# Kernel optimization log

Measured on AMD Instinct MI355X. Metric: run time of the kernel, lower is better.

Reference implementation:

```python
import jax, jax.numpy as jnp
import numpy as np

N_QUBITS = 8
N_LAYERS = 2
BATCH = 16384
DIM = 2 ** N_QUBITS

# PauliZ sign table: Z[q, idx] = +1 if bit q of idx is 0 else -1 (qubit 0 = MSB,
# matching state axis ordering below).
_bits = (np.arange(DIM)[:, None] >> (N_QUBITS - 1 - np.arange(N_QUBITS))) & 1
Z_SIGNS = jnp.asarray((1 - 2 * _bits).T.astype(np.float32))  # (n_qubits, 2^n)


def _apply_1q(state, gates, q):
    """Apply batched single-qubit gate. state: (B,)+(2,)*n complex, gates: (B,2,2)."""
    s = jnp.moveaxis(state, 1 + q, -1)
    s = jnp.einsum('nab,...b->...a', gates, s.reshape(gates.shape[0], -1, 2).reshape(s.shape))
    # the einsum above: gates (B,2,2) broadcast over the intermediate axes
    return jnp.moveaxis(s, -1, 1 + q)


def _apply_1q_batched(state, gates, q):
    s = jnp.moveaxis(state, 1 + q, -1)          # (B, ..., 2)
    s = jnp.einsum('nab,n...b->n...a', gates, s)
    return jnp.moveaxis(s, -1, 1 + q)


def _apply_cnot(state, c, t):
    s = jnp.moveaxis(state, (1 + c, 1 + t), (-2, -1))  # (..., 2_ctrl, 2_tgt)
    s = jnp.concatenate([s[..., :1, :], s[..., 1:, ::-1]], axis=-2)  # flip target where ctrl=1
    return jnp.moveaxis(s, (-2, -1), (1 + c, 1 + t))


def _rx_gate(theta):
    """Batched RX(theta): (B,) -> (B,2,2) complex."""
    c = jnp.cos(theta / 2)
    s = -1j * jnp.sin(theta / 2)
    return jnp.stack([jnp.stack([c + 0j, s], -1), jnp.stack([s, c + 0j], -1)], -2)


def _rot_gate(phi, theta, omega):
    """PennyLane Rot(phi,theta,omega) = RZ(omega) RY(theta) RZ(phi). Batched (B,)->(B,2,2)."""
    c = jnp.cos(theta / 2)
    s = jnp.sin(theta / 2)
    ep = jnp.exp(-0.5j * (phi + omega))  # e^{-i(phi+omega)/2}
    em = jnp.exp(0.5j * (phi - omega))   # e^{ i(phi-omega)/2}
    m00 = ep * c
    m01 = -em * s
    m10 = jnp.conj(em) * s
    m11 = jnp.conj(ep) * c
    return jnp.stack([jnp.stack([m00, m01], -1), jnp.stack([m10, m11], -1)], -2)


def _circuit(inputs, hidden):
    B = inputs.shape[0]
    n = N_QUBITS
    state = jnp.zeros((B,) + (2,) * n, jnp.complex64)
    state = state.at[(slice(None),) + (0,) * n].set(1.0 + 0j)
    # AngleEmbedding: RX(inputs[:, q]) on each wire q
    for q in range(n):
        state = _apply_1q_batched(state, _rx_gate(inputs[:, q]), q)
    # n_layers calls of StronglyEntanglingLayers, each with 1 layer of weights
    for l in range(N_LAYERS):
        w = hidden[:, l, 0]  # (B, n_qubits, 3)
        for q in range(n):
            state = _apply_1q_batched(state, _rot_gate(w[:, q, 0], w[:, q, 1], w[:, q, 2]), q)
        for q in range(n):  # CNOT ring, range r = 1
            state = _apply_cnot(state, q, (q + 1) % n)
    probs = jnp.abs(state.reshape(B, DIM)) ** 2          # (B, 2^n)
    expvals = probs @ Z_SIGNS.T                          # (B, n_qubits) <Z_q>
    return jnp.tanh(expvals)


def setup_inputs() -> dict:
    key = jax.random.key(0)
    k1, k2 = jax.random.split(key)
    inputs = jax.random.normal(k1, (BATCH, N_QUBITS), dtype=jnp.float32)
    hidden = jax.random.normal(k2, (BATCH, N_LAYERS, 1, N_QUBITS, 3), dtype=jnp.float32)
    return {"inputs": inputs, "hidden": hidden}


def reference(inputs, hidden):
    h = _circuit(inputs, hidden)
    return (h, h)
```

## Files before the change

kernel.cpp:

```cpp
#include <hip/hip_runtime.h>
#include <math.h>


#define DEVINL __device__ __forceinline__

DEVINL void fast_sincos_half(float x, float& s, float& c) {
    const float r = x * 0.07957747154594767f;
    s = __builtin_amdgcn_sinf(r);
    c = __builtin_amdgcn_cosf(r);
}

DEVINL float fast_tanh(float x) {
    const float t = __builtin_amdgcn_exp2f(x * 2.8853900817779268f);
    return 1.0f - 2.0f * __builtin_amdgcn_rcpf(t + 1.0f);
}

DEVINL void cmul(float ar, float ai, float br, float bi, float& cr, float& ci) {
    cr = ar*br - ai*bi;
    ci = ar*bi + ai*br;
}
DEVINL void cmulc(float ar, float ai, float br, float bi, float& cr, float& ci) {
    cr = ar*br + ai*bi;
    ci = ar*bi - ai*br;
}

template<int CTRL>
DEVINL float dpp_perm(float x) {
    return __int_as_float(__builtin_amdgcn_update_dpp(
        __float_as_int(x), __float_as_int(x), CTRL, 0xF, 0xF, false));
}

template<int OFF>
DEVINL float swz(float x) {
    return __int_as_float(__builtin_amdgcn_ds_swizzle(__float_as_int(x), OFF));
}

DEVINL void qubit_vec(float x, float phi, float theta, float omega,
                      float& v0r, float& v0i, float& v1r, float& v1i)
{
    float s, c;   fast_sincos_half(x, s, c);
    float st, ct; fast_sincos_half(theta, st, ct);
    float sa, ca; fast_sincos_half(phi + omega, sa, ca);
    float sb, cb; fast_sincos_half(phi - omega, sb, cb);
    const float A = c*ct, B = s*st, C = c*st, D = s*ct;
    v0r = ca*A - sb*B;
    v0i = cb*B - sa*A;
    v1r = cb*C + sa*D;
    v1i = -(sb*C + ca*D);
}

__global__ __launch_bounds__(256, 8)
void qcirc_kernel(const float* __restrict__ inputs,
                  const float* __restrict__ hidden,
                  float* __restrict__ out, int B)
{
    __shared__ __align__(16) float lds[512];

    const int t  = threadIdx.x;
    const int e  = blockIdx.x * 8 + (t >> 5);
    if (e >= B) return;
    const int sl = t & 31;
    const int gb = t & 32;
    const int q  = sl & 7;
    const int eb = (t >> 5) * 64;
    const int sl0 = sl & 1, sl1 = (sl >> 1) & 1, sl2 = (sl >> 2) & 1,
              sl3 = (sl >> 3) & 1, sl4 = (sl >> 4) & 1;

    const float  x  = inputs[(size_t)e * 8 + q];
    const float* hb = hidden + (size_t)e * 48 + q * 3;
    const float ph1 = hb[0], th1 = hb[1], om1 = hb[2];
    const float ph2 = hb[24], th2 = hb[25];

    float ov0r, ov0i, ov1r, ov1i;
    qubit_vec(x, ph1, th1, om1, ov0r, ov0i, ov1r, ov1i);
    float s2o, c2o; fast_sincos_half(th2, s2o, c2o);
    const float ho = ph2 * 0.07957747154594767f;
    const float Ec = __builtin_amdgcn_cosf(ho);
    const float Es = __builtin_amdgcn_sinf(ho);
    const float Av = (q < 3) ? Ec : ho;
    const float Bv = (q < 3) ? Es : 0.f;

    if (sl < 8) {
        *(float4*)(lds + eb + q*8)     = make_float4(ov0r, ov0i, ov1r, ov1i);
        *(float4*)(lds + eb + q*8 + 4) = make_float4(c2o, s2o, Av, Bv);
    }

    const float4 r4v = *(const float4*)(lds + eb + 32);
    const float4 r5v = *(const float4*)(lds + eb + 40);
    const float4 r6v = *(const float4*)(lds + eb + 48);
    const float4 r7v = *(const float4*)(lds + eb + 56);
    const int s4 = sl3 ^ sl4, s5 = sl2 ^ sl3, s6 = sl1, s7 = sl0 ^ sl1;
    const float a4r = s4 ? r4v.z : r4v.x, a4i = s4 ? r4v.w : r4v.y;
    const float a5r = s5 ? r5v.z : r5v.x, a5i = s5 ? r5v.w : r5v.y;
    const float a6r = s6 ? r6v.z : r6v.x, a6i = s6 ? r6v.w : r6v.y;
    const float a7r = s7 ? r7v.z : r7v.x, a7i = s7 ? r7v.w : r7v.y;
    float Lr, Li, tr, ti;
    cmul(a4r, a4i, a5r, a5i, tr, ti);
    cmul(tr, ti, a6r, a6i, Lr, Li);
    cmul(Lr, Li, a7r, a7i, tr, ti); Lr = tr; Li = ti;

    {
        const float h3 = lds[eb + 3*8 + 6];
        const float h4 = lds[eb + 4*8 + 6];
        const float h5 = lds[eb + 5*8 + 6];
        const float h6 = lds[eb + 6*8 + 6];
        const float h7 = lds[eb + 7*8 + 6];
        const float lam = (sl4 ? h3 : -h3) + (sl3 ? h4 : -h4) + (sl2 ? h5 : -h5)
                        + ((sl1 ^ sl2) ? h6 : -h6) + ((sl0 ^ sl2) ? h7 : -h7);
        const float Pc = __builtin_amdgcn_cosf(lam);
        const float Ps = __builtin_amdgcn_sinf(lam);
        cmul(Lr, Li, Pc, Ps, tr, ti); Lr = tr; Li = ti;
    }

    const float2 E0 = *(const float2*)(lds + eb + 0*8 + 6);
    const float2 E1 = *(const float2*)(lds + eb + 1*8 + 6);
    const float2 E2 = *(const float2*)(lds + eb + 2*8 + 6);

    const float4 r0v = *(const float4*)(lds + eb + 0);
    const float4 r1v = *(const float4*)(lds + eb + 8);
    const float4 r2v = *(const float4*)(lds + eb + 16);
    const float4 r3v = *(const float4*)(lds + eb + 24);

    const int b01 = sl0 ^ sl2;
    const float w0r0 = b01 ? r0v.z : r0v.x, w0i0 = b01 ? r0v.w : r0v.y;
    const float w0r1 = b01 ? r0v.x : r0v.z, w0i1 = b01 ? r0v.y : r0v.w;
    const float w1r0 = b01 ? r1v.z : r1v.x, w1i0 = b01 ? r1v.w : r1v.y;
    const float w1r1 = b01 ? r1v.x : r1v.z, w1i1 = b01 ? r1v.y : r1v.w;
    const float w3r0 = sl4 ? r3v.z : r3v.x, w3i0 = sl4 ? r3v.w : r3v.y;
    const float w3r1 = sl4 ? r3v.x : r3v.z, w3i1 = sl4 ? r3v.y : r3v.w;

    float w3p0r, w3p0i, w3p1r, w3p1i;
    cmulc(E2.x, E2.y, w3r0, w3i0, w3p0r, w3p0i);
    cmul (w3r1, w3i1, E2.x, E2.y, w3p1r, w3p1i);

    float GL0r, GL0i, GL1r, GL1i, GL2r, GL2i, GL3r, GL3i;
    {
        const float a = E0.x*E1.x, b2 = E0.y*E1.y, c = E0.x*E1.y, d = E0.y*E1.x;
        const float P3r = a - b2, P3i = c + d;
        const float P1r = a + b2, P1i = c - d;
        cmulc(P3r, P3i, Lr, Li, GL0r, GL0i);
        cmul (P1r, P1i, Lr, Li, GL1r, GL1i);
        cmulc(P1r, P1i, Lr, Li, GL2r, GL2i);
        cmul (P3r, P3i, Lr, Li, GL3r, GL3i);
    }

    float T2r[4], T2i[4], T1r[4], T1i[4];
    cmul(w0r0, w0i0, w1r0, w1i0, tr, ti); cmul(tr, ti, GL0r, GL0i, T2r[0], T2i[0]);
    cmul(w0r0, w0i0, w1r1, w1i1, tr, ti); cmul(tr, ti, GL1r, GL1i, T2r[1], T2i[1]);
    cmul(w0r1, w0i1, w1r1, w1i1, tr, ti); cmul(tr, ti, GL2r, GL2i, T2r[2], T2i[2]);
    cmul(w0r1, w0i1, w1r0, w1i0, tr, ti); cmul(tr, ti, GL3r, GL3i, T2r[3], T2i[3]);
    cmul(r2v.x, r2v.y, w3p0r, w3p0i, T1r[0], T1i[0]);
    cmul(r2v.z, r2v.w, w3p1r, w3p1i, T1r[1], T1i[1]);
    cmul(r2v.z, r2v.w, w3p0r, w3p0i, T1r[2], T1i[2]);
    cmul(r2v.x, r2v.y, w3p1r, w3p1i, T1r[3], T1i[3]);

    {
        const float2 cs = *(const float2*)(lds + eb + 0*8 + 4);
        #pragma unroll
        for (int j = 0; j < 2; ++j) {
            const float lr = T2r[j], li = T2i[j], hr = T2r[j+2], hi = T2i[j+2];
            T2r[j]   = cs.x*lr - cs.y*hr;  T2i[j]   = cs.x*li - cs.y*hi;
            T2r[j+2] = cs.y*lr + cs.x*hr;  T2i[j+2] = cs.y*li + cs.x*hi;
        }
    }
    {
        const float2 cs = *(const float2*)(lds + eb + 2*8 + 4);
        #pragma unroll
        for (int j = 0; j < 4; j += 2) {
            const float lr = T1r[j], li = T1i[j], hr = T1r[j+1], hi = T1i[j+1];
            T1r[j]   = cs.x*lr - cs.y*hr;  T1i[j]   = cs.x*li - cs.y*hi;
            T1r[j+1] = cs.y*lr + cs.x*hr;  T1i[j+1] = cs.y*li + cs.x*hi;
        }
    }

    float ar[8], ai[8];
    #pragma unroll
    for (int k = 0; k < 8; ++k)
        cmul(T2r[k >> 1], T2i[k >> 1], T1r[k & 3], T1i[k & 3], ar[k], ai[k]);

    {
        const float2 cs = *(const float2*)(lds + eb + 1*8 + 4);
        #pragma unroll
        for (int k0 = 0; k0 < 8; ++k0) {
            if (k0 & 2) continue;
            const int k1 = k0 | 2;
            const float lr = ar[k0], li = ai[k0], hr = ar[k1], hi = ai[k1];
            ar[k0] = cs.x*lr - cs.y*hr;  ai[k0] = cs.x*li - cs.y*hi;
            ar[k1] = cs.y*lr + cs.x*hr;  ai[k1] = cs.y*li + cs.x*hi;
        }
    }
    {
        const float2 cs = *(const float2*)(lds + eb + 3*8 + 4);
        const float se = sl4 ? cs.y : -cs.y;
        #pragma unroll
        for (int k = 0; k < 8; ++k) {
            const float pr = swz<0x401F>(ar[k]);
            const float pi = swz<0x401F>(ai[k]);
            ar[k] = cs.x*ar[k] + se*pr;
            ai[k] = cs.x*ai[k] + se*pi;
        }
    }
    {
        const float2 cs = *(const float2*)(lds + eb + 4*8 + 4);
        const float se = sl3 ? cs.y : -cs.y;
        #pragma unroll
        for (int k = 0; k < 8; ++k) {
            ar[k] = cs.x*ar[k] + se*dpp_perm<0x128>(ar[k]);
            ai[k] = cs.x*ai[k] + se*dpp_perm<0x128>(ai[k]);
        }
    }
    {
        const float2 cs = *(const float2*)(lds + eb + 5*8 + 4);
        const float se = sl2 ? cs.y : -cs.y;
        #pragma unroll
        for (int k = 0; k < 8; ++k) {
            ar[k] = cs.x*ar[k] + se*dpp_perm<0x141>(ar[k]);
            ai[k] = cs.x*ai[k] + se*dpp_perm<0x141>(ai[k]);
        }
    }
    {
        const float2 cs = *(const float2*)(lds + eb + 6*8 + 4);
        const float se = (sl1 ^ sl2) ? cs.y : -cs.y;
        #pragma unroll
        for (int k = 0; k < 8; ++k) {
            ar[k] = cs.x*ar[k] + se*dpp_perm<0x4E>(ar[k]);
            ai[k] = cs.x*ai[k] + se*dpp_perm<0x4E>(ai[k]);
        }
    }
    {
        const float2 cs = *(const float2*)(lds + eb + 7*8 + 4);
        const float se = (sl0 ^ sl2) ? cs.y : -cs.y;
        #pragma unroll
        for (int k = 0; k < 8; ++k) {
            ar[k] = cs.x*ar[k] + se*dpp_perm<0xB1>(ar[k]);
            ai[k] = cs.x*ai[k] + se*dpp_perm<0xB1>(ai[k]);
        }
    }

    float P[8];
    #pragma unroll
    for (int k = 0; k < 8; ++k) P[k] = ar[k]*ar[k] + ai[k]*ai[k];
    const float u0 = P[0]+P[1], v0 = P[0]-P[1];
    const float u1 = P[2]+P[3], v1 = P[2]-P[3];
    const float u2 = P[4]+P[5], v2 = P[4]-P[5];
    const float u3 = P[6]+P[7], v3 = P[6]-P[7];
    float V3 = v0 - v1 + v2 - v3;
    float V6 = u0 - u1 - u2 + u3;
    float V7 = v0 - v1 - v2 + v3;

    {
        const float g1 = (sl & 1) ? -1.f : 1.f;
        V3 = fmaf(g1, V3, dpp_perm<0xB1>(V3));
        V6 = fmaf(g1, V6, dpp_perm<0xB1>(V6));
        V7 = fmaf(g1, V7, dpp_perm<0xB1>(V7));
        const float g2 = (sl & 2) ? -1.f : 1.f;
        V3 = fmaf(g2, V3, dpp_perm<0x4E>(V3));
        V6 = fmaf(g2, V6, dpp_perm<0x4E>(V6));
        V7 = fmaf(g2, V7, dpp_perm<0x4E>(V7));
        const float g4 = (sl & 4) ? -1.f : 1.f;
        V3 = fmaf(g4, V3, swz<0x101F>(V3));
        V6 = fmaf(g4, V6, swz<0x101F>(V6));
        V7 = fmaf(g4, V7, swz<0x101F>(V7));
        const float g8 = (sl & 8) ? -1.f : 1.f;
        V3 = fmaf(g8, V3, dpp_perm<0x128>(V3));
        V6 = fmaf(g8, V6, dpp_perm<0x128>(V6));
        V7 = fmaf(g8, V7, dpp_perm<0x128>(V7));
        const float g16 = (sl & 16) ? -1.f : 1.f;
        V3 = fmaf(g16, V3, swz<0x401F>(V3));
        V6 = fmaf(g16, V6, swz<0x401F>(V6));
        V7 = fmaf(g16, V7, swz<0x401F>(V7));
    }

    const int idx7 = (sl == 3) ? 16 : (sl == 4) ? 24 : (sl == 5) ? 28
                   : (sl == 6) ? 26 : (sl == 7) ? 31 : 0;
    const float B3 = swz<0x3E0>(V3);
    const float B6 = swz<0x000>(V6);
    const float B7 = __shfl(V7, gb + idx7, 64);
    const float rsel = (sl == 0) ? B3 : (sl == 1) ? B6 : B7;
    const float h = fast_tanh(rsel);
    if (sl < 8) {
        const size_t obase = (size_t)e * 8;
        out[obase + sl] = h;
        out[(size_t)B * 8 + obase + sl] = h;
    }
}

extern "C" void kernel_launch(void* const* d_in, const int* in_sizes, int n_in,
                              void* d_out, int out_size, void* d_ws, size_t ws_size,
                              hipStream_t stream)
{
    const float* inputs = (const float*)d_in[0];
    const float* hidden = (const float*)d_in[1];
    float* out = (float*)d_out;
    const int B = in_sizes[0] / 8;
    const int blocks = (B + 7) / 8;
    hipLaunchKernelGGL(qcirc_kernel, dim3(blocks), dim3(256), 0, stream,
                       inputs, hidden, out, B);
}
```

Measured before the change: 13.53 us.

## Map each batch element to 16 lanes holding 16 amplitudes per lane

Each circuit instance now runs on 16 lanes instead of 32, and each lane holds 16 complex amplitudes instead of 8. Qubit 3 is therefore applied in registers rather than through a cross-lane swizzle, and one butterfly stage of the final reduction disappears. The qubit-4 swizzle in the reduction becomes a pair of DPP ops, and the final result gather is reorganised to match. This halves the lanes per element and removes ds_swizzle traffic, at the cost of twice the registers per lane (launch bounds are lowered from 8 to 4 blocks) and possibly lower occupancy.

```diff
diff --git a/kernel.cpp b/kernel.cpp
--- a/kernel.cpp
+++ b/kernel.cpp
@@ -16,12 +16,10 @@
 }
 
 DEVINL void cmul(float ar, float ai, float br, float bi, float& cr, float& ci) {
-    cr = ar*br - ai*bi;
-    ci = ar*bi + ai*br;
+    cr = ar*br - ai*bi;  ci = ar*bi + ai*br;
 }
 DEVINL void cmulc(float ar, float ai, float br, float bi, float& cr, float& ci) {
-    cr = ar*br + ai*bi;
-    ci = ar*bi - ai*br;
+    cr = ar*br + ai*bi;  ci = ar*bi - ai*br;
 }
 
 template<int CTRL>
@@ -29,7 +27,6 @@
     return __int_as_float(__builtin_amdgcn_update_dpp(
         __float_as_int(x), __float_as_int(x), CTRL, 0xF, 0xF, false));
 }
-
 template<int OFF>
 DEVINL float swz(float x) {
     return __int_as_float(__builtin_amdgcn_ds_swizzle(__float_as_int(x), OFF));
@@ -43,28 +40,25 @@
     float sa, ca; fast_sincos_half(phi + omega, sa, ca);
     float sb, cb; fast_sincos_half(phi - omega, sb, cb);
     const float A = c*ct, B = s*st, C = c*st, D = s*ct;
-    v0r = ca*A - sb*B;
-    v0i = cb*B - sa*A;
-    v1r = cb*C + sa*D;
-    v1i = -(sb*C + ca*D);
-}
-
-__global__ __launch_bounds__(256, 8)
+    v0r = ca*A - sb*B;  v0i = cb*B - sa*A;
+    v1r = cb*C + sa*D;  v1i = -(sb*C + ca*D);
+}
+
+__global__ __launch_bounds__(256, 4)
 void qcirc_kernel(const float* __restrict__ inputs,
                   const float* __restrict__ hidden,
                   float* __restrict__ out, int B)
 {
-    __shared__ __align__(16) float lds[512];
+    __shared__ __align__(16) float lds[1024];
 
     const int t  = threadIdx.x;
-    const int e  = blockIdx.x * 8 + (t >> 5);
+    const int e  = blockIdx.x * 16 + (t >> 4);
     if (e >= B) return;
-    const int sl = t & 31;
-    const int gb = t & 32;
+    const int sl = t & 15;
     const int q  = sl & 7;
-    const int eb = (t >> 5) * 64;
+    const int eb = (t >> 4) * 64;
     const int sl0 = sl & 1, sl1 = (sl >> 1) & 1, sl2 = (sl >> 2) & 1,
-              sl3 = (sl >> 3) & 1, sl4 = (sl >> 4) & 1;
+              sl3 = (sl >> 3) & 1;
 
     const float  x  = inputs[(size_t)e * 8 + q];
     const float* hb = hidden + (size_t)e * 48 + q * 3;
@@ -77,134 +71,142 @@
     const float ho = ph2 * 0.07957747154594767f;
     const float Ec = __builtin_amdgcn_cosf(ho);
     const float Es = __builtin_amdgcn_sinf(ho);
-    const float Av = (q < 3) ? Ec : ho;
-    const float Bv = (q < 3) ? Es : 0.f;
+    const float Av = (q < 4) ? Ec : ho;
+    const float Bv = (q < 4) ? Es : 0.f;
 
     if (sl < 8) {
         *(float4*)(lds + eb + q*8)     = make_float4(ov0r, ov0i, ov1r, ov1i);
         *(float4*)(lds + eb + q*8 + 4) = make_float4(c2o, s2o, Av, Bv);
     }
 
-    const float4 r4v = *(const float4*)(lds + eb + 32);
-    const float4 r5v = *(const float4*)(lds + eb + 40);
-    const float4 r6v = *(const float4*)(lds + eb + 48);
-    const float4 r7v = *(const float4*)(lds + eb + 56);
-    const int s4 = sl3 ^ sl4, s5 = sl2 ^ sl3, s6 = sl1, s7 = sl0 ^ sl1;
-    const float a4r = s4 ? r4v.z : r4v.x, a4i = s4 ? r4v.w : r4v.y;
-    const float a5r = s5 ? r5v.z : r5v.x, a5i = s5 ? r5v.w : r5v.y;
-    const float a6r = s6 ? r6v.z : r6v.x, a6i = s6 ? r6v.w : r6v.y;
-    const float a7r = s7 ? r7v.z : r7v.x, a7i = s7 ? r7v.w : r7v.y;
-    float Lr, Li, tr, ti;
-    cmul(a4r, a4i, a5r, a5i, tr, ti);
-    cmul(tr, ti, a6r, a6i, Lr, Li);
-    cmul(Lr, Li, a7r, a7i, tr, ti); Lr = tr; Li = ti;
-
-    {
-        const float h3 = lds[eb + 3*8 + 6];
+    float Lr, Li;
+    {
+        const float4 r5 = *(const float4*)(lds + eb + 40);
+        const float4 r6 = *(const float4*)(lds + eb + 48);
+        const float4 r7 = *(const float4*)(lds + eb + 56);
+        const int s5 = sl2 ^ sl3, s6 = sl1, s7 = sl0 ^ sl1;
+        const float a5r = s5 ? r5.z : r5.x, a5i = s5 ? r5.w : r5.y;
+        const float a6r = s6 ? r6.z : r6.x, a6i = s6 ? r6.w : r6.y;
+        const float a7r = s7 ? r7.z : r7.x, a7i = s7 ? r7.w : r7.y;
+        float tr, ti;
+        cmul(a5r, a5i, a6r, a6i, tr, ti);
+        cmul(tr, ti, a7r, a7i, Lr, Li);
+    }
+    {
         const float h4 = lds[eb + 4*8 + 6];
         const float h5 = lds[eb + 5*8 + 6];
         const float h6 = lds[eb + 6*8 + 6];
         const float h7 = lds[eb + 7*8 + 6];
-        const float lam = (sl4 ? h3 : -h3) + (sl3 ? h4 : -h4) + (sl2 ? h5 : -h5)
+        const float lam = (sl3 ? h4 : -h4) + (sl2 ? h5 : -h5)
                         + ((sl1 ^ sl2) ? h6 : -h6) + ((sl0 ^ sl2) ? h7 : -h7);
         const float Pc = __builtin_amdgcn_cosf(lam);
         const float Ps = __builtin_amdgcn_sinf(lam);
-        cmul(Lr, Li, Pc, Ps, tr, ti); Lr = tr; Li = ti;
-    }
-
-    const float2 E0 = *(const float2*)(lds + eb + 0*8 + 6);
-    const float2 E1 = *(const float2*)(lds + eb + 1*8 + 6);
-    const float2 E2 = *(const float2*)(lds + eb + 2*8 + 6);
-
-    const float4 r0v = *(const float4*)(lds + eb + 0);
-    const float4 r1v = *(const float4*)(lds + eb + 8);
-    const float4 r2v = *(const float4*)(lds + eb + 16);
-    const float4 r3v = *(const float4*)(lds + eb + 24);
-
-    const int b01 = sl0 ^ sl2;
-    const float w0r0 = b01 ? r0v.z : r0v.x, w0i0 = b01 ? r0v.w : r0v.y;
-    const float w0r1 = b01 ? r0v.x : r0v.z, w0i1 = b01 ? r0v.y : r0v.w;
-    const float w1r0 = b01 ? r1v.z : r1v.x, w1i0 = b01 ? r1v.w : r1v.y;
-    const float w1r1 = b01 ? r1v.x : r1v.z, w1i1 = b01 ? r1v.y : r1v.w;
-    const float w3r0 = sl4 ? r3v.z : r3v.x, w3i0 = sl4 ? r3v.w : r3v.y;
-    const float w3r1 = sl4 ? r3v.x : r3v.z, w3i1 = sl4 ? r3v.y : r3v.w;
-
-    float w3p0r, w3p0i, w3p1r, w3p1i;
-    cmulc(E2.x, E2.y, w3r0, w3i0, w3p0r, w3p0i);
-    cmul (w3r1, w3i1, E2.x, E2.y, w3p1r, w3p1i);
-
-    float GL0r, GL0i, GL1r, GL1i, GL2r, GL2i, GL3r, GL3i;
-    {
-        const float a = E0.x*E1.x, b2 = E0.y*E1.y, c = E0.x*E1.y, d = E0.y*E1.x;
-        const float P3r = a - b2, P3i = c + d;
-        const float P1r = a + b2, P1i = c - d;
-        cmulc(P3r, P3i, Lr, Li, GL0r, GL0i);
-        cmul (P1r, P1i, Lr, Li, GL1r, GL1i);
-        cmulc(P1r, P1i, Lr, Li, GL2r, GL2i);
-        cmul (P3r, P3i, Lr, Li, GL3r, GL3i);
-    }
-
-    float T2r[4], T2i[4], T1r[4], T1i[4];
-    cmul(w0r0, w0i0, w1r0, w1i0, tr, ti); cmul(tr, ti, GL0r, GL0i, T2r[0], T2i[0]);
-    cmul(w0r0, w0i0, w1r1, w1i1, tr, ti); cmul(tr, ti, GL1r, GL1i, T2r[1], T2i[1]);
-    cmul(w0r1, w0i1, w1r1, w1i1, tr, ti); cmul(tr, ti, GL2r, GL2i, T2r[2], T2i[2]);
-    cmul(w0r1, w0i1, w1r0, w1i0, tr, ti); cmul(tr, ti, GL3r, GL3i, T2r[3], T2i[3]);
-    cmul(r2v.x, r2v.y, w3p0r, w3p0i, T1r[0], T1i[0]);
-    cmul(r2v.z, r2v.w, w3p1r, w3p1i, T1r[1], T1i[1]);
-    cmul(r2v.z, r2v.w, w3p0r, w3p0i, T1r[2], T1i[2]);
-    cmul(r2v.x, r2v.y, w3p1r, w3p1i, T1r[3], T1i[3]);
-
-    {
-        const float2 cs = *(const float2*)(lds + eb + 0*8 + 4);
+        float tr, ti; cmul(Lr, Li, Pc, Ps, tr, ti); Lr = tr; Li = ti;
+    }
+
+    float Ur[4], Ui[4];
+    {
+        const float4 r0 = *(const float4*)(lds + eb + 0);
+        const float4 r1 = *(const float4*)(lds + eb + 8);
+        const float2 E0 = *(const float2*)(lds + eb + 0*8 + 6);
+        const float2 E1 = *(const float2*)(lds + eb + 1*8 + 6);
+        const int b01 = sl0 ^ sl2;
+        const float w00r = b01 ? r0.z : r0.x, w00i = b01 ? r0.w : r0.y;
+        const float w01r = b01 ? r0.x : r0.z, w01i = b01 ? r0.y : r0.w;
+        const float w10r = b01 ? r1.z : r1.x, w10i = b01 ? r1.w : r1.y;
+        const float w11r = b01 ? r1.x : r1.z, w11i = b01 ? r1.y : r1.w;
+        const float aa = E0.x*E1.x, bb = E0.y*E1.y, cc = E0.x*E1.y, dd = E0.y*E1.x;
+        const float P3r = aa - bb, P3i = cc + dd;
+        const float P1r = aa + bb, P1i = cc - dd;
+        float tr, ti;
+        cmul(w00r,w00i, w10r,w10i, tr,ti); cmulc(P3r,P3i, tr,ti, Ur[0],Ui[0]);
+        cmul(w00r,w00i, w11r,w11i, tr,ti); cmul (P1r,P1i, tr,ti, Ur[1],Ui[1]);
+        cmul(w01r,w01i, w11r,w11i, tr,ti); cmulc(P1r,P1i, tr,ti, Ur[2],Ui[2]);
+        cmul(w01r,w01i, w10r,w10i, tr,ti); cmul (P3r,P3i, tr,ti, Ur[3],Ui[3]);
+        const float2 cs0 = *(const float2*)(lds + eb + 0*8 + 4);
         #pragma unroll
         for (int j = 0; j < 2; ++j) {
-            const float lr = T2r[j], li = T2i[j], hr = T2r[j+2], hi = T2i[j+2];
-            T2r[j]   = cs.x*lr - cs.y*hr;  T2i[j]   = cs.x*li - cs.y*hi;
-            T2r[j+2] = cs.y*lr + cs.x*hr;  T2i[j+2] = cs.y*li + cs.x*hi;
-        }
-    }
-    {
-        const float2 cs = *(const float2*)(lds + eb + 2*8 + 4);
+            const float lr = Ur[j], li = Ui[j], hr = Ur[j+2], hi = Ui[j+2];
+            Ur[j]   = cs0.x*lr - cs0.y*hr;  Ui[j]   = cs0.x*li - cs0.y*hi;
+            Ur[j+2] = cs0.y*lr + cs0.x*hr;  Ui[j+2] = cs0.y*li + cs0.x*hi;
+        }
+    }
+
+    float T2r[8], T2i[8];
+    {
+        const float4 r2 = *(const float4*)(lds + eb + 16);
+        #pragma unroll
+        for (int m = 0; m < 8; ++m) {
+            const int idx = (m & 1) ^ ((m >> 1) & 1);
+            const float vr = idx ? r2.z : r2.x;
+            const float vi = idx ? r2.w : r2.y;
+            cmul(Ur[m >> 1], Ui[m >> 1], vr, vi, T2r[m], T2i[m]);
+        }
+        const float2 cs1 = *(const float2*)(lds + eb + 1*8 + 4);
+        #pragma unroll
+        for (int m = 0; m < 8; ++m) {
+            if (m & 2) continue;
+            const int m1 = m | 2;
+            const float lr = T2r[m], li = T2i[m], hr = T2r[m1], hi = T2i[m1];
+            T2r[m]  = cs1.x*lr - cs1.y*hr;  T2i[m]  = cs1.x*li - cs1.y*hi;
+            T2r[m1] = cs1.y*lr + cs1.x*hr;  T2i[m1] = cs1.y*li + cs1.x*hi;
+        }
+    }
+
+    float T1r[4], T1i[4];
+    {
+        const float4 r3 = *(const float4*)(lds + eb + 24);
+        const float4 r4 = *(const float4*)(lds + eb + 32);
+        const float2 E2 = *(const float2*)(lds + eb + 2*8 + 6);
+        const float2 E3 = *(const float2*)(lds + eb + 3*8 + 6);
+        const float w40r = sl3 ? r4.z : r4.x, w40i = sl3 ? r4.w : r4.y;
+        const float w41r = sl3 ? r4.x : r4.z, w41i = sl3 ? r4.y : r4.w;
+        float D0r, D0i, D1r, D1i;
+        cmulc(E3.x, E3.y, w40r, w40i, D0r, D0i);
+        cmul (w41r, w41i, E3.x, E3.y, D1r, D1i);
+        float LD0r, LD0i, LD1r, LD1i;
+        cmul(D0r, D0i, Lr, Li, LD0r, LD0i);
+        cmul(D1r, D1i, Lr, Li, LD1r, LD1i);
+        float e00r,e00i, e01r,e01i, e10r,e10i, e11r,e11i;
+        cmulc(E2.x, E2.y, r3.x, r3.y, e00r, e00i);
+        cmulc(E2.x, E2.y, r3.z, r3.w, e01r, e01i);
+        cmul (r3.z, r3.w, E2.x, E2.y, e10r, e10i);
+        cmul (r3.x, r3.y, E2.x, E2.y, e11r, e11i);
+        cmul(e00r, e00i, LD0r, LD0i, T1r[0], T1i[0]);
+        cmul(e01r, e01i, LD1r, LD1i, T1r[1], T1i[1]);
+        cmul(e10r, e10i, LD0r, LD0i, T1r[2], T1i[2]);
+        cmul(e11r, e11i, LD1r, LD1i, T1r[3], T1i[3]);
+        const float2 cs3 = *(const float2*)(lds + eb + 3*8 + 4);
         #pragma unroll
         for (int j = 0; j < 4; j += 2) {
             const float lr = T1r[j], li = T1i[j], hr = T1r[j+1], hi = T1i[j+1];
-            T1r[j]   = cs.x*lr - cs.y*hr;  T1i[j]   = cs.x*li - cs.y*hi;
-            T1r[j+1] = cs.y*lr + cs.x*hr;  T1i[j+1] = cs.y*li + cs.x*hi;
-        }
-    }
-
-    float ar[8], ai[8];
+            T1r[j]   = cs3.x*lr - cs3.y*hr;  T1i[j]   = cs3.x*li - cs3.y*hi;
+            T1r[j+1] = cs3.y*lr + cs3.x*hr;  T1i[j+1] = cs3.y*li + cs3.x*hi;
+        }
+    }
+
+    float ar[16], ai[16];
     #pragma unroll
-    for (int k = 0; k < 8; ++k)
+    for (int k = 0; k < 16; ++k)
         cmul(T2r[k >> 1], T2i[k >> 1], T1r[k & 3], T1i[k & 3], ar[k], ai[k]);
 
     {
-        const float2 cs = *(const float2*)(lds + eb + 1*8 + 4);
-        #pragma unroll
-        for (int k0 = 0; k0 < 8; ++k0) {
-            if (k0 & 2) continue;
-            const int k1 = k0 | 2;
-            const float lr = ar[k0], li = ai[k0], hr = ar[k1], hi = ai[k1];
-            ar[k0] = cs.x*lr - cs.y*hr;  ai[k0] = cs.x*li - cs.y*hi;
+        const float2 cs = *(const float2*)(lds + eb + 2*8 + 4);
+        #pragma unroll
+        for (int k = 0; k < 16; ++k) {
+            if (k & 2) continue;
+            const int k1 = k | 2;
+            const float lr = ar[k], li = ai[k], hr = ar[k1], hi = ai[k1];
+            ar[k]  = cs.x*lr - cs.y*hr;  ai[k]  = cs.x*li - cs.y*hi;
             ar[k1] = cs.y*lr + cs.x*hr;  ai[k1] = cs.y*li + cs.x*hi;
         }
     }
-    {
-        const float2 cs = *(const float2*)(lds + eb + 3*8 + 4);
-        const float se = sl4 ? cs.y : -cs.y;
-        #pragma unroll
-        for (int k = 0; k < 8; ++k) {
-            const float pr = swz<0x401F>(ar[k]);
-            const float pi = swz<0x401F>(ai[k]);
-            ar[k] = cs.x*ar[k] + se*pr;
-            ai[k] = cs.x*ai[k] + se*pi;
-        }
-    }
+
     {
         const float2 cs = *(const float2*)(lds + eb + 4*8 + 4);
         const float se = sl3 ? cs.y : -cs.y;
         #pragma unroll
-        for (int k = 0; k < 8; ++k) {
+        for (int k = 0; k < 16; ++k) {
             ar[k] = cs.x*ar[k] + se*dpp_perm<0x128>(ar[k]);
             ai[k] = cs.x*ai[k] + se*dpp_perm<0x128>(ai[k]);
         }
@@ -213,7 +215,7 @@
         const float2 cs = *(const float2*)(lds + eb + 5*8 + 4);
         const float se = sl2 ? cs.y : -cs.y;
         #pragma unroll
-        for (int k = 0; k < 8; ++k) {
+        for (int k = 0; k < 16; ++k) {
             ar[k] = cs.x*ar[k] + se*dpp_perm<0x141>(ar[k]);
             ai[k] = cs.x*ai[k] + se*dpp_perm<0x141>(ai[k]);
         }
@@ -222,7 +224,7 @@
         const float2 cs = *(const float2*)(lds + eb + 6*8 + 4);
         const float se = (sl1 ^ sl2) ? cs.y : -cs.y;
         #pragma unroll
-        for (int k = 0; k < 8; ++k) {
+        for (int k = 0; k < 16; ++k) {
             ar[k] = cs.x*ar[k] + se*dpp_perm<0x4E>(ar[k]);
             ai[k] = cs.x*ai[k] + se*dpp_perm<0x4E>(ai[k]);
         }
@@ -231,52 +233,66 @@
         const float2 cs = *(const float2*)(lds + eb + 7*8 + 4);
         const float se = (sl0 ^ sl2) ? cs.y : -cs.y;
         #pragma unroll
-        for (int k = 0; k < 8; ++k) {
+        for (int k = 0; k < 16; ++k) {
             ar[k] = cs.x*ar[k] + se*dpp_perm<0xB1>(ar[k]);
             ai[k] = cs.x*ai[k] + se*dpp_perm<0xB1>(ai[k]);
         }
     }
 
-    float P[8];
+    float P[16];
     #pragma unroll
-    for (int k = 0; k < 8; ++k) P[k] = ar[k]*ar[k] + ai[k]*ai[k];
-    const float u0 = P[0]+P[1], v0 = P[0]-P[1];
-    const float u1 = P[2]+P[3], v1 = P[2]-P[3];
-    const float u2 = P[4]+P[5], v2 = P[4]-P[5];
-    const float u3 = P[6]+P[7], v3 = P[6]-P[7];
-    float V3 = v0 - v1 + v2 - v3;
-    float V6 = u0 - u1 - u2 + u3;
-    float V7 = v0 - v1 - v2 + v3;
+    for (int k = 0; k < 16; ++k) P[k] = ar[k]*ar[k] + ai[k]*ai[k];
+
+    float A_[8], D_[8];
+    #pragma unroll
+    for (int j = 0; j < 8; ++j) {
+        A_[j] = P[2*j] + P[2*j+1];
+        D_[j] = P[2*j] - P[2*j+1];
+    }
+    float DD[4], AD[4], AA[4];
+    #pragma unroll
+    for (int j = 0; j < 4; ++j) {
+        DD[j] = D_[2*j] - D_[2*j+1];
+        AD[j] = A_[2*j] - A_[2*j+1];
+        AA[j] = A_[2*j] + A_[2*j+1];
+    }
+    const float G0  = DD[0] - DD[1], G1  = DD[2] - DD[3];
+    const float GE0 = AD[0] - AD[1], GE1 = AD[2] - AD[3];
+    const float GC0 = AA[0] - AA[1], GC1 = AA[2] - AA[3];
+    float V7k = G0 + G1;
+    float VFk = G0 - G1;
+    float VEk = GE0 - GE1;
+    float VCk = GC0 - GC1;
 
     {
         const float g1 = (sl & 1) ? -1.f : 1.f;
-        V3 = fmaf(g1, V3, dpp_perm<0xB1>(V3));
-        V6 = fmaf(g1, V6, dpp_perm<0xB1>(V6));
-        V7 = fmaf(g1, V7, dpp_perm<0xB1>(V7));
+        V7k = fmaf(g1, V7k, dpp_perm<0xB1>(V7k));
+        VCk = fmaf(g1, VCk, dpp_perm<0xB1>(VCk));
+        VEk = fmaf(g1, VEk, dpp_perm<0xB1>(VEk));
+        VFk = fmaf(g1, VFk, dpp_perm<0xB1>(VFk));
         const float g2 = (sl & 2) ? -1.f : 1.f;
-        V3 = fmaf(g2, V3, dpp_perm<0x4E>(V3));
-        V6 = fmaf(g2, V6, dpp_perm<0x4E>(V6));
-        V7 = fmaf(g2, V7, dpp_perm<0x4E>(V7));
+        V7k = fmaf(g2, V7k, dpp_perm<0x4E>(V7k));
+        VCk = fmaf(g2, VCk, dpp_perm<0x4E>(VCk));
+        VEk = fmaf(g2, VEk, dpp_perm<0x4E>(VEk));
+        VFk = fmaf(g2, VFk, dpp_perm<0x4E>(VFk));
         const float g4 = (sl & 4) ? -1.f : 1.f;
-        V3 = fmaf(g4, V3, swz<0x101F>(V3));
-        V6 = fmaf(g4, V6, swz<0x101F>(V6));
-        V7 = fmaf(g4, V7, swz<0x101F>(V7));
+        V7k = fmaf(g4, V7k, dpp_perm<0x1B>(dpp_perm<0x141>(V7k)));
+        VCk = fmaf(g4, VCk, dpp_perm<0x1B>(dpp_perm<0x141>(VCk)));
+        VEk = fmaf(g4, VEk, dpp_perm<0x1B>(dpp_perm<0x141>(VEk)));
+        VFk = fmaf(g4, VFk, dpp_perm<0x1B>(dpp_perm<0x141>(VFk)));
         const float g8 = (sl & 8) ? -1.f : 1.f;
-        V3 = fmaf(g8, V3, dpp_perm<0x128>(V3));
-        V6 = fmaf(g8, V6, dpp_perm<0x128>(V6));
-        V7 = fmaf(g8, V7, dpp_perm<0x128>(V7));
-        const float g16 = (sl & 16) ? -1.f : 1.f;
-        V3 = fmaf(g16, V3, swz<0x401F>(V3));
-        V6 = fmaf(g16, V6, swz<0x401F>(V6));
-        V7 = fmaf(g16, V7, swz<0x401F>(V7));
-    }
-
-    const int idx7 = (sl == 3) ? 16 : (sl == 4) ? 24 : (sl == 5) ? 28
-                   : (sl == 6) ? 26 : (sl == 7) ? 31 : 0;
-    const float B3 = swz<0x3E0>(V3);
-    const float B6 = swz<0x000>(V6);
-    const float B7 = __shfl(V7, gb + idx7, 64);
-    const float rsel = (sl == 0) ? B3 : (sl == 1) ? B6 : B7;
+        V7k = fmaf(g8, V7k, dpp_perm<0x128>(V7k));
+        VCk = fmaf(g8, VCk, dpp_perm<0x128>(VCk));
+        VEk = fmaf(g8, VEk, dpp_perm<0x128>(VEk));
+        VFk = fmaf(g8, VFk, dpp_perm<0x128>(VFk));
+    }
+
+    const float B7 = swz<0x1F0>(V7k);
+    const float BC = swz<0x010>(VCk);
+    const float BE = swz<0x010>(VEk);
+    const int idx = (int)((0xFAC80000u >> ((sl & 7) * 4)) & 0xFu);
+    const float BF = __shfl(VFk, (t & 0x30) | idx, 64);
+    const float rsel = (sl == 0) ? B7 : (sl == 1) ? BC : (sl == 2) ? BE : BF;
     const float h = fast_tanh(rsel);
     if (sl < 8) {
         const size_t obase = (size_t)e * 8;
@@ -293,7 +309,7 @@
     const float* hidden = (const float*)d_in[1];
     float* out = (float*)d_out;
     const int B = in_sizes[0] / 8;
-    const int blocks = (B + 7) / 8;
+    const int blocks = (B + 15) / 16;
     hipLaunchKernelGGL(qcirc_kernel, dim3(blocks), dim3(256), 0, stream,
                        inputs, hidden, out, B);
 }
```

After: 12.59 us, median of 2. 6.9% less time.
